# Optimization experiments

Hardware: AMD Instinct MI355X
Metric: run time of the kernel (lower is better)

## Reference

```python
import jax, jax.numpy as jnp
import numpy as np
import math

HEAD_DIM = 128
THETA = 10000.0
MASK_VAL = -10000.0


def _rope(x, cos, sin):
    # x: (B, S, D); cos/sin: (S, D//2). Pairs (even, odd) rotated as complex.
    xr = x.reshape(*x.shape[:-1], -1, 2)
    xe, xo = xr[..., 0], xr[..., 1]
    oe = xe * cos - xo * sin
    oo = xe * sin + xo * cos
    return jnp.stack([oe, oo], axis=-1).reshape(x.shape)


def setup_inputs() -> dict:
    key = jax.random.key(0)
    B, S, D = 8, 4096, HEAD_DIM
    qkv = jax.random.normal(key, (B, S, 3 * D), dtype=jnp.float32)
    return {"qkv": qkv}


def reference(qkv):
    B, S, threeD = qkv.shape
    D = threeD // 3
    qkv = qkv.reshape(B, S, 3, D)
    q, k, v = qkv[:, :, 0], qkv[:, :, 1], qkv[:, :, 2]

    # precompute_freqs_cis: outer(t, 1/theta^(2i/d)) -> cos/sin (S, D//2)
    inv_freq = 1.0 / (THETA ** (jnp.arange(0, D, 2, dtype=jnp.float32) / D))
    freqs = jnp.arange(S, dtype=jnp.float32)[:, None] * inv_freq[None, :]
    cos, sin = jnp.cos(freqs), jnp.sin(freqs)
    q = _rope(q, cos, sin)
    k = _rope(k, cos, sin)

    scale = 1.0 / math.sqrt(D)
    scores = jnp.einsum('btd,bsd->bts', q, k) * scale  # (B, S, S)
    causal_mask = jnp.triu(jnp.full((S, S), MASK_VAL, dtype=scores.dtype), 1)
    attn = jax.nn.softmax(scores + causal_mask, axis=-1)
    out = jnp.einsum('bts,bsd->btd', attn, v)  # (B, S, D)
    return out
```

## Files before the change

kernel.cpp:

```cpp
#include <hip/hip_runtime.h>
#include <math.h>

typedef _Float16 half8 __attribute__((ext_vector_type(8)));
typedef float floatx4 __attribute__((ext_vector_type(4)));
typedef float floatx2 __attribute__((ext_vector_type(2)));

#define B_ 8
#define S_ 4096
#define SCALE_L2E 0.12751743008389106f
#define MASK_L2E  -14426.950408889634f
#define L2_10K_OVER_128 0.10381025296522975f

#define PLD 72
#define KW  136
#define VW  24
#define OSTLD 136
#define SLOTS_PER_B 576
#define NW 8
#define KVTILE 8192

__device__ __forceinline__ int chunk_prefix(int qt32) {
    int g = qt32 >> 4;
    return qt32 + 8 * g * (g - 1) + (qt32 - (g << 4)) * g;
}

__device__ __forceinline__ void glds16(const _Float16* src, _Float16* dst) {
    __builtin_amdgcn_global_load_lds((const __attribute__((address_space(1))) void*)src,
                                     (__attribute__((address_space(3))) void*)dst, 16, 0, 0);
}

__global__ __launch_bounds__(256) void prep_kernel(const float* __restrict__ qkv,
                                                   _Float16* __restrict__ Qh,
                                                   _Float16* __restrict__ Kp,
                                                   _Float16* __restrict__ Vp) {
    __shared__ __align__(16) _Float16 Kl[16][KW];
    __shared__ __align__(16) _Float16 Vt[128][VW];
    const int tid = threadIdx.x;
    const int b   = blockIdx.y;
    const int s0  = blockIdx.x * 16;

#pragma unroll
    for (int it = 0; it < 4; ++it) {
        int idx = tid + it * 256;
        int i = idx & 63, sr = idx >> 6, s = s0 + sr;
        const float* base = qkv + ((size_t)(b * S_ + s)) * 384 + 2 * i;
        floatx2 q2 = *(const floatx2*)base;
        floatx2 k2 = *(const floatx2*)(base + 128);
        float inv = exp2f(-(float)(2 * i) * L2_10K_OVER_128);
        float ang = (float)s * inv;
        float sn, cs;
        __sincosf(ang, &sn, &cs);
        size_t oq = ((size_t)(b * S_ + s)) * 128 + 2 * i;
        Qh[oq]     = (_Float16)((q2[0] * cs - q2[1] * sn) * SCALE_L2E);
        Qh[oq + 1] = (_Float16)((q2[0] * sn + q2[1] * cs) * SCALE_L2E);
        Kl[sr][2 * i]     = (_Float16)(k2[0] * cs - k2[1] * sn);
        Kl[sr][2 * i + 1] = (_Float16)(k2[0] * sn + k2[1] * cs);
    }
#pragma unroll
    for (int it = 0; it < 2; ++it) {
        int idx = tid + it * 256;
        int c = idx & 31, sr = idx >> 5;
        floatx4 v = *(const floatx4*)(qkv + ((size_t)(b * S_ + s0 + sr)) * 384 + 256 + c * 4);
#pragma unroll
        for (int j = 0; j < 4; ++j) Vt[c * 4 + j][sr] = (_Float16)v[j];
    }
    __syncthreads();

    {
        int c = tid >> 6, lane = tid & 63;
        int quad = lane >> 4, n = lane & 15;
        half8 val = *(const half8*)&Kl[n][c * 32 + quad * 8];
        int s16 = s0 >> 4;
        *(half8*)(Kp + (((size_t)(b * 256 + s16) * 4 + c) * 64 + lane) * 8) = val;
    }
    {
        int kt = s0 >> 6, c2 = (s0 >> 5) & 1, qp = (s0 >> 4) & 1;
        int nt = tid >> 5, lq = (tid >> 4) & 1, n = tid & 15;
        int quad = qp * 2 + lq;
        int lane = quad * 16 + n;
        half8 val = *(const half8*)&Vt[nt * 16 + n][lq * 8];
        *(half8*)(Vp + ((((size_t)(b * 64 + kt) * 2 + c2) * 8 + nt) * 64 + lane) * 8) = val;
    }
}

__global__ __launch_bounds__(512) void attn_part_kernel(const _Float16* __restrict__ Qh,
                                                        const _Float16* __restrict__ Kp,
                                                        const _Float16* __restrict__ Vp,
                                                        _Float16* __restrict__ Ppart,
                                                        float* __restrict__ Lpart) {
    __shared__ __align__(16) _Float16 KVs[2][2][KVTILE];
    __shared__ __align__(16) _Float16 Psh[NW][4 * 16 * PLD];

    const int tid  = threadIdx.x;
    const int w    = tid >> 6;
    const int lane = tid & 63;
    const int quad = lane >> 4;
    const int l16  = lane & 15;
    const int b     = blockIdx.x & 7;
    const int chunk = blockIdx.x >> 3;
    const int c0    = chunk * 8;

    const int qt32_top  = 127 - blockIdx.y * 8;
    const int ktmax_blk = (qt32_top * 32 + 31) >> 6;
    if (c0 > ktmax_blk) return;
    const int kend_blk  = min(ktmax_blk, c0 + 7);

    const int qt32   = qt32_top - w;
    const int qr0    = qt32 * 32;
    const int kt_max = (qr0 + 31) >> 6;
    const bool has_work = (c0 <= kt_max);
    const int kend   = min(kt_max, c0 + 7);
    const int slot   = b * SLOTS_PER_B + chunk_prefix(qt32) + chunk;
    _Float16* SHw = &Psh[w][0];

    half8 aq[2][4];
#pragma unroll
    for (int tile = 0; tile < 2; ++tile) {
        const _Float16* Qb = Qh + ((size_t)(b * S_) + qr0 + tile * 16 + l16) * 128;
#pragma unroll
        for (int c = 0; c < 4; ++c) aq[tile][c] = *(const half8*)(Qb + c * 32 + quad * 8);
    }

    floatx4 o[2][8];
#pragma unroll
    for (int tile = 0; tile < 2; ++tile)
#pragma unroll
        for (int i = 0; i < 8; ++i) o[tile][i] = (floatx4){0.f, 0.f, 0.f, 0.f};
    float rsum[2][4] = {{0.f, 0.f, 0.f, 0.f}, {0.f, 0.f, 0.f, 0.f}};

    const _Float16* Kb = Kp + (size_t)b * 524288;
    const _Float16* Vb = Vp + (size_t)b * 524288;

    {
        const _Float16* ks = Kb + (size_t)c0 * KVTILE + (w * 2) * 512 + lane * 8;
        const _Float16* vs = Vb + (size_t)c0 * KVTILE + (w * 2) * 512 + lane * 8;
        _Float16* kd = &KVs[c0 & 1][0][(w * 2) * 512];
        _Float16* vd = &KVs[c0 & 1][1][(w * 2) * 512];
        glds16(ks, kd);       glds16(vs, vd);
        glds16(ks + 512, kd + 512); glds16(vs + 512, vd + 512);
    }

    for (int kt = c0; kt <= kend_blk; ++kt) {
        const int buf = kt & 1;
        if (kt < kend_blk) {
            const _Float16* ks = Kb + (size_t)(kt + 1) * KVTILE + (w * 2) * 512 + lane * 8;
            const _Float16* vs = Vb + (size_t)(kt + 1) * KVTILE + (w * 2) * 512 + lane * 8;
            _Float16* kd = &KVs[buf ^ 1][0][(w * 2) * 512];
            _Float16* vd = &KVs[buf ^ 1][1][(w * 2) * 512];
            glds16(ks, kd);       glds16(vs, vd);
            glds16(ks + 512, kd + 512); glds16(vs + 512, vd + 512);
            asm volatile("s_waitcnt vmcnt(4)" ::: "memory");
        } else {
            asm volatile("s_waitcnt vmcnt(0)" ::: "memory");
        }
        __builtin_amdgcn_s_barrier();

        if (has_work && kt <= kend) {
            const _Float16* Klds = &KVs[buf][0][0];
            const _Float16* Vlds = &KVs[buf][1][0];

            floatx4 s4[2][4];
#pragma unroll
            for (int t = 0; t < 4; ++t) {
                half8 bk[4];
#pragma unroll
                for (int c = 0; c < 4; ++c)
                    bk[c] = *(const half8*)&Klds[((t * 4 + c) * 64 + lane) * 8];
                floatx4 a0 = (floatx4){0.f, 0.f, 0.f, 0.f};
                floatx4 a1 = (floatx4){0.f, 0.f, 0.f, 0.f};
                __builtin_amdgcn_s_setprio(1);
#pragma unroll
                for (int c = 0; c < 4; ++c) {
                    a0 = __builtin_amdgcn_mfma_f32_16x16x32_f16(aq[0][c], bk[c], a0, 0, 0, 0);
                    a1 = __builtin_amdgcn_mfma_f32_16x16x32_f16(aq[1][c], bk[c], a1, 0, 0, 0);
                }
                __builtin_amdgcn_s_setprio(0);
                s4[0][t] = a0; s4[1][t] = a1;
            }

            if (kt == kt_max) {
#pragma unroll
                for (int tile = 0; tile < 2; ++tile)
#pragma unroll
                    for (int t = 0; t < 4; ++t)
#pragma unroll
                        for (int r = 0; r < 4; ++r) {
                            int kcol = kt * 64 + t * 16 + l16;
                            int qr   = qr0 + tile * 16 + quad * 4 + r;
                            if (kcol > qr) s4[tile][t][r] += MASK_L2E;
                        }
            }

#pragma unroll
            for (int tile = 0; tile < 2; ++tile)
#pragma unroll
                for (int t = 0; t < 4; ++t)
#pragma unroll
                    for (int r = 0; r < 4; ++r) {
                        float p = __builtin_amdgcn_exp2f(s4[tile][t][r]);
                        rsum[tile][r] += p;
                        SHw[(tile * 2 + buf) * (16 * PLD) + (quad * 4 + r) * PLD + t * 16 + l16] = (_Float16)p;
                    }

#pragma unroll
            for (int c2 = 0; c2 < 2; ++c2) {
                half8 vf[8];
#pragma unroll
                for (int nt = 0; nt < 8; ++nt)
                    vf[nt] = *(const half8*)&Vlds[((c2 * 8 + nt) * 64 + lane) * 8];
#pragma unroll
                for (int tile = 0; tile < 2; ++tile) {
                    half8 ap = *(const half8*)&SHw[(tile * 2 + buf) * (16 * PLD) + l16 * PLD + c2 * 32 + quad * 8];
                    __builtin_amdgcn_s_setprio(1);
#pragma unroll
                    for (int nt = 0; nt < 8; ++nt)
                        o[tile][nt] = __builtin_amdgcn_mfma_f32_16x16x32_f16(ap, vf[nt], o[tile][nt], 0, 0, 0);
                    __builtin_amdgcn_s_setprio(0);
                }
            }
        }
        asm volatile("" ::: "memory");
        __builtin_amdgcn_s_barrier();
    }

    if (!has_work) return;

#pragma unroll
    for (int off = 1; off <= 8; off <<= 1)
#pragma unroll
        for (int tile = 0; tile < 2; ++tile)
#pragma unroll
            for (int r = 0; r < 4; ++r)
                rsum[tile][r] += __shfl_xor(rsum[tile][r], off, 64);
    if (l16 == 0) {
#pragma unroll
        for (int tile = 0; tile < 2; ++tile)
#pragma unroll
            for (int r = 0; r < 4; ++r)
                Lpart[(size_t)slot * 32 + tile * 16 + quad * 4 + r] = rsum[tile][r];
    }

    _Float16* Ost = SHw;
#pragma unroll
    for (int tile = 0; tile < 2; ++tile)
#pragma unroll
        for (int nt = 0; nt < 8; ++nt)
#pragma unroll
            for (int r = 0; r < 4; ++r)
                Ost[(tile * 16 + quad * 4 + r) * OSTLD + nt * 16 + l16] = (_Float16)o[tile][nt][r];
    _Float16* pp = Ppart + (size_t)slot * 4096;
#pragma unroll
    for (int i = 0; i < 8; ++i) {
        int idx = lane + i * 64;
        half8 v = *(const half8*)&Ost[(idx >> 4) * OSTLD + (idx & 15) * 8];
        *(half8*)(pp + (size_t)idx * 8) = v;
    }
}

__global__ __launch_bounds__(256) void reduce_kernel(const _Float16* __restrict__ Ppart,
                                                     const float* __restrict__ Lpart,
                                                     float* __restrict__ out) {
    const int bid  = blockIdx.x;
    const int b    = bid >> 7;
    const int qt32 = bid & 127;
    const int qr0  = qt32 * 32;
    const int nch  = (((qr0 + 31) >> 6) >> 3) + 1;
    const int slot0 = b * SLOTS_PER_B + chunk_prefix(qt32);
    const _Float16* pp = Ppart + (size_t)slot0 * 4096;
    const float* lp = Lpart + (size_t)slot0 * 32;
    const int tid = threadIdx.x;

#pragma unroll
    for (int j = 0; j < 2; ++j) {
        int idx = tid + j * 256;
        int row = idx >> 4;
        float acc[8] = {0.f, 0.f, 0.f, 0.f, 0.f, 0.f, 0.f, 0.f};
        float l = 0.f;
        for (int c = 0; c < nch; ++c) {
            half8 v = *(const half8*)(pp + (size_t)c * 4096 + (size_t)idx * 8);
#pragma unroll
            for (int k = 0; k < 8; ++k) acc[k] += (float)v[k];
            l += lp[c * 32 + row];
        }
        float inv = 1.0f / l;
        float* ob = out + ((size_t)(b * S_) + qr0) * 128 + (size_t)idx * 8;
        floatx4 o0 = (floatx4){acc[0] * inv, acc[1] * inv, acc[2] * inv, acc[3] * inv};
        floatx4 o1 = (floatx4){acc[4] * inv, acc[5] * inv, acc[6] * inv, acc[7] * inv};
        *(floatx4*)ob = o0;
        *(floatx4*)(ob + 4) = o1;
    }
}

__global__ __launch_bounds__(64) void attn_atomic_kernel(const _Float16* __restrict__ Qh,
                                                         const _Float16* __restrict__ Kp,
                                                         const _Float16* __restrict__ Vp,
                                                         float* __restrict__ out,
                                                         float* __restrict__ Lg) {
    __shared__ __align__(16) _Float16 Pl[2][16 * PLD];
    const int lane = threadIdx.x, quad = lane >> 4, l16 = lane & 15;
    const int b = blockIdx.x & 7, chunk = blockIdx.x >> 3;
    const int qt = 255 - blockIdx.y, qr0 = qt * 16;
    const int kt_max = qt >> 2, c0 = chunk * 8;
    if (c0 > kt_max) return;
    const int kend = min(kt_max, c0 + 7);
    const _Float16* Qb = Qh + ((size_t)(b * S_) + qr0 + l16) * 128;
    half8 aq[4];
#pragma unroll
    for (int c = 0; c < 4; ++c) aq[c] = *(const half8*)(Qb + c * 32 + quad * 8);
    floatx4 o[8];
#pragma unroll
    for (int i = 0; i < 8; ++i) o[i] = (floatx4){0.f, 0.f, 0.f, 0.f};
    float rsum[4] = {0.f, 0.f, 0.f, 0.f};
    const _Float16* Kb = Kp + (size_t)b * 524288;
    const _Float16* Vb = Vp + (size_t)b * 524288;
    for (int kt = c0; kt <= kend; ++kt) {
        half8 vf[2][8];
#pragma unroll
        for (int c2 = 0; c2 < 2; ++c2)
#pragma unroll
            for (int nt = 0; nt < 8; ++nt)
                vf[c2][nt] = *(const half8*)(Vb + (((size_t)(kt * 2 + c2) * 8 + nt) * 64 + lane) * 8);
        floatx4 s4[4];
#pragma unroll
        for (int t = 0; t < 4; ++t) {
            const _Float16* kp = Kb + ((size_t)((kt * 4 + t) * 4) * 64 + lane) * 8;
            floatx4 acc = (floatx4){0.f, 0.f, 0.f, 0.f};
#pragma unroll
            for (int c = 0; c < 4; ++c) {
                half8 bk = *(const half8*)(kp + c * 512);
                acc = __builtin_amdgcn_mfma_f32_16x16x32_f16(aq[c], bk, acc, 0, 0, 0);
            }
            s4[t] = acc;
        }
        if (kt == kt_max) {
#pragma unroll
            for (int t = 0; t < 4; ++t)
#pragma unroll
                for (int r = 0; r < 4; ++r) {
                    int kcol = kt * 64 + t * 16 + l16;
                    int qr = qr0 + quad * 4 + r;
                    if (kcol > qr) s4[t][r] += MASK_L2E;
                }
        }
        const int buf = kt & 1;
#pragma unroll
        for (int t = 0; t < 4; ++t)
#pragma unroll
            for (int r = 0; r < 4; ++r) {
                float p = __builtin_amdgcn_exp2f(s4[t][r]);
                rsum[r] += p;
                Pl[buf][(quad * 4 + r) * PLD + t * 16 + l16] = (_Float16)p;
            }
#pragma unroll
        for (int c2 = 0; c2 < 2; ++c2) {
            half8 ap = *(const half8*)&Pl[buf][l16 * PLD + c2 * 32 + quad * 8];
#pragma unroll
            for (int nt = 0; nt < 8; ++nt)
                o[nt] = __builtin_amdgcn_mfma_f32_16x16x32_f16(ap, vf[c2][nt], o[nt], 0, 0, 0);
        }
    }
#pragma unroll
    for (int off = 1; off <= 8; off <<= 1)
#pragma unroll
        for (int r = 0; r < 4; ++r)
            rsum[r] += __shfl_xor(rsum[r], off, 64);
    if (l16 == 0) {
#pragma unroll
        for (int r = 0; r < 4; ++r)
            atomicAdd(&Lg[(size_t)(b * S_) + qr0 + quad * 4 + r], rsum[r]);
    }
    float* ob = out + ((size_t)(b * S_) + qr0) * 128;
#pragma unroll
    for (int nt = 0; nt < 8; ++nt)
#pragma unroll
        for (int r = 0; r < 4; ++r)
            atomicAdd(&ob[(quad * 4 + r) * 128 + nt * 16 + l16], o[nt][r]);
}

__global__ __launch_bounds__(256) void norm_kernel(float* __restrict__ out,
                                                   const float* __restrict__ Lg) {
    int i = blockIdx.x * 256 + threadIdx.x;
    int row = i >> 5;
    floatx4 v = *(floatx4*)(out + (size_t)i * 4);
    float inv = 1.0f / Lg[row];
    v[0] *= inv; v[1] *= inv; v[2] *= inv; v[3] *= inv;
    *(floatx4*)(out + (size_t)i * 4) = v;
}

extern "C" void kernel_launch(void* const* d_in, const int* in_sizes, int n_in,
                              void* d_out, int out_size, void* d_ws, size_t ws_size,
                              hipStream_t stream) {
    const float* qkv = (const float*)d_in[0];
    float* out = (float*)d_out;
    const size_t MB = 1024 * 1024;
    _Float16* Qh = (_Float16*)d_ws;
    _Float16* Kp = (_Float16*)((char*)d_ws + 8 * MB);
    _Float16* Vp = (_Float16*)((char*)d_ws + 16 * MB);

    const size_t lpart_bytes = (size_t)B_ * SLOTS_PER_B * 32 * sizeof(float);
    const size_t ppart_bytes = (size_t)B_ * SLOTS_PER_B * 4096 * sizeof(_Float16);
    const size_t need = 25 * MB + ppart_bytes;

    prep_kernel<<<dim3(256, B_), dim3(256), 0, stream>>>(qkv, Qh, Kp, Vp);

    if (ws_size >= need) {
        float*    Lpart = (float*)((char*)d_ws + 24 * MB);
        _Float16* Ppart = (_Float16*)((char*)d_ws + 25 * MB);
        (void)lpart_bytes;
        attn_part_kernel<<<dim3(64, 16), dim3(512), 0, stream>>>(Qh, Kp, Vp, Ppart, Lpart);
        reduce_kernel<<<dim3(1024), dim3(256), 0, stream>>>(Ppart, Lpart, out);
    } else {
        float* Lg = (float*)((char*)d_ws + 24 * MB);
        hipMemsetAsync(out, 0, (size_t)B_ * S_ * 128 * sizeof(float), stream);
        hipMemsetAsync(Lg, 0, (size_t)B_ * S_ * sizeof(float), stream);
        attn_atomic_kernel<<<dim3(64, 256), dim3(64), 0, stream>>>(Qh, Kp, Vp, out, Lg);
        norm_kernel<<<dim3(4096), dim3(256), 0, stream>>>(out, Lg);
    }
}
```

Measured before the change: 165.0 us.

## Halve KV tile to 32 keys and pool LDS to raise attention occupancy

Result: no change. 164.7 us (-0.1%).

```diff
diff --git a/kernel.cpp b/kernel.cpp
--- a/kernel.cpp
+++ b/kernel.cpp
@@ -11,13 +11,13 @@
 #define MASK_L2E  -14426.950408889634f
 #define L2_10K_OVER_128 0.10381025296522975f
 
-#define PLD 72
+#define PLD2 40
 #define KW  136
 #define VW  24
 #define OSTLD 136
 #define SLOTS_PER_B 576
 #define NW 8
-#define KVTILE 8192
+#define POOL_HALFS (16384 + NW * 2 * 16 * PLD2)
 
 __device__ __forceinline__ int chunk_prefix(int qt32) {
     int g = qt32 >> 4;
@@ -88,8 +88,7 @@
                                                         const _Float16* __restrict__ Vp,
                                                         _Float16* __restrict__ Ppart,
                                                         float* __restrict__ Lpart) {
-    __shared__ __align__(16) _Float16 KVs[2][2][KVTILE];
-    __shared__ __align__(16) _Float16 Psh[NW][4 * 16 * PLD];
+    __shared__ __align__(16) _Float16 POOL[POOL_HALFS];
 
     const int tid  = threadIdx.x;
     const int w    = tid >> 6;
@@ -111,7 +110,7 @@
     const bool has_work = (c0 <= kt_max);
     const int kend   = min(kt_max, c0 + 7);
     const int slot   = b * SLOTS_PER_B + chunk_prefix(qt32) + chunk;
-    _Float16* SHw = &Psh[w][0];
+    _Float16* Pw = POOL + 16384 + w * (2 * 16 * PLD2);
 
     half8 aq[2][4];
 #pragma unroll
@@ -131,41 +130,42 @@
     const _Float16* Kb = Kp + (size_t)b * 524288;
     const _Float16* Vb = Vp + (size_t)b * 524288;
 
+    const int ht0    = 2 * c0;
+    const int ht_end = 2 * kend_blk + 1;
+
     {
-        const _Float16* ks = Kb + (size_t)c0 * KVTILE + (w * 2) * 512 + lane * 8;
-        const _Float16* vs = Vb + (size_t)c0 * KVTILE + (w * 2) * 512 + lane * 8;
-        _Float16* kd = &KVs[c0 & 1][0][(w * 2) * 512];
-        _Float16* vd = &KVs[c0 & 1][1][(w * 2) * 512];
-        glds16(ks, kd);       glds16(vs, vd);
-        glds16(ks + 512, kd + 512); glds16(vs + 512, vd + 512);
-    }
-
-    for (int kt = c0; kt <= kend_blk; ++kt) {
-        const int buf = kt & 1;
-        if (kt < kend_blk) {
-            const _Float16* ks = Kb + (size_t)(kt + 1) * KVTILE + (w * 2) * 512 + lane * 8;
-            const _Float16* vs = Vb + (size_t)(kt + 1) * KVTILE + (w * 2) * 512 + lane * 8;
-            _Float16* kd = &KVs[buf ^ 1][0][(w * 2) * 512];
-            _Float16* vd = &KVs[buf ^ 1][1][(w * 2) * 512];
-            glds16(ks, kd);       glds16(vs, vd);
-            glds16(ks + 512, kd + 512); glds16(vs + 512, vd + 512);
-            asm volatile("s_waitcnt vmcnt(4)" ::: "memory");
+        const _Float16* ks = Kb + (size_t)ht0 * 4096 + w * 512 + lane * 8;
+        const _Float16* vs = Vb + (size_t)ht0 * 4096 + w * 512 + lane * 8;
+        glds16(ks, POOL + w * 512);
+        glds16(vs, POOL + 4096 + w * 512);
+    }
+
+    for (int ht = ht0; ht <= ht_end; ++ht) {
+        const int buf = ht & 1;
+        if (ht < ht_end) {
+            const _Float16* ks = Kb + (size_t)(ht + 1) * 4096 + w * 512 + lane * 8;
+            const _Float16* vs = Vb + (size_t)(ht + 1) * 4096 + w * 512 + lane * 8;
+            _Float16* kd = POOL + (buf ^ 1) * 8192 + w * 512;
+            glds16(ks, kd);
+            glds16(vs, kd + 4096);
+            asm volatile("s_waitcnt vmcnt(2)" ::: "memory");
         } else {
             asm volatile("s_waitcnt vmcnt(0)" ::: "memory");
         }
         __builtin_amdgcn_s_barrier();
 
+        const int kt = ht >> 1, h = ht & 1;
         if (has_work && kt <= kend) {
-            const _Float16* Klds = &KVs[buf][0][0];
-            const _Float16* Vlds = &KVs[buf][1][0];
-
-            floatx4 s4[2][4];
-#pragma unroll
-            for (int t = 0; t < 4; ++t) {
+            const _Float16* Klds = POOL + buf * 8192;
+            const _Float16* Vlds = Klds + 4096;
+
+            floatx4 s4[2][2];
+#pragma unroll
+            for (int tl = 0; tl < 2; ++tl) {
                 half8 bk[4];
 #pragma unroll
                 for (int c = 0; c < 4; ++c)
-                    bk[c] = *(const half8*)&Klds[((t * 4 + c) * 64 + lane) * 8];
+                    bk[c] = *(const half8*)&Klds[((tl * 4 + c) * 64 + lane) * 8];
                 floatx4 a0 = (floatx4){0.f, 0.f, 0.f, 0.f};
                 floatx4 a1 = (floatx4){0.f, 0.f, 0.f, 0.f};
                 __builtin_amdgcn_s_setprio(1);
@@ -175,42 +175,41 @@
                     a1 = __builtin_amdgcn_mfma_f32_16x16x32_f16(aq[1][c], bk[c], a1, 0, 0, 0);
                 }
                 __builtin_amdgcn_s_setprio(0);
-                s4[0][t] = a0; s4[1][t] = a1;
+                s4[0][tl] = a0; s4[1][tl] = a1;
             }
 
             if (kt == kt_max) {
 #pragma unroll
                 for (int tile = 0; tile < 2; ++tile)
 #pragma unroll
-                    for (int t = 0; t < 4; ++t)
+                    for (int tl = 0; tl < 2; ++tl)
 #pragma unroll
                         for (int r = 0; r < 4; ++r) {
-                            int kcol = kt * 64 + t * 16 + l16;
+                            int kcol = kt * 64 + h * 32 + tl * 16 + l16;
                             int qr   = qr0 + tile * 16 + quad * 4 + r;
-                            if (kcol > qr) s4[tile][t][r] += MASK_L2E;
+                            if (kcol > qr) s4[tile][tl][r] += MASK_L2E;
                         }
             }
 
 #pragma unroll
             for (int tile = 0; tile < 2; ++tile)
 #pragma unroll
-                for (int t = 0; t < 4; ++t)
+                for (int tl = 0; tl < 2; ++tl)
 #pragma unroll
                     for (int r = 0; r < 4; ++r) {
-                        float p = __builtin_amdgcn_exp2f(s4[tile][t][r]);
+                        float p = __builtin_amdgcn_exp2f(s4[tile][tl][r]);
                         rsum[tile][r] += p;
-                        SHw[(tile * 2 + buf) * (16 * PLD) + (quad * 4 + r) * PLD + t * 16 + l16] = (_Float16)p;
+                        Pw[tile * (16 * PLD2) + (quad * 4 + r) * PLD2 + tl * 16 + l16] = (_Float16)p;
                     }
 
-#pragma unroll
-            for (int c2 = 0; c2 < 2; ++c2) {
+            {
                 half8 vf[8];
 #pragma unroll
                 for (int nt = 0; nt < 8; ++nt)
-                    vf[nt] = *(const half8*)&Vlds[((c2 * 8 + nt) * 64 + lane) * 8];
+                    vf[nt] = *(const half8*)&Vlds[(nt * 64 + lane) * 8];
 #pragma unroll
                 for (int tile = 0; tile < 2; ++tile) {
-                    half8 ap = *(const half8*)&SHw[(tile * 2 + buf) * (16 * PLD) + l16 * PLD + c2 * 32 + quad * 8];
+                    half8 ap = *(const half8*)&Pw[tile * (16 * PLD2) + l16 * PLD2 + quad * 8];
                     __builtin_amdgcn_s_setprio(1);
 #pragma unroll
                     for (int nt = 0; nt < 8; ++nt)
@@ -240,20 +239,22 @@
                 Lpart[(size_t)slot * 32 + tile * 16 + quad * 4 + r] = rsum[tile][r];
     }
 
-    _Float16* Ost = SHw;
-#pragma unroll
-    for (int tile = 0; tile < 2; ++tile)
+    asm volatile("" ::: "memory");
+    _Float16* Ost = POOL + w * (POOL_HALFS / NW);
+    _Float16* pp = Ppart + (size_t)slot * 4096;
+#pragma unroll
+    for (int tile = 0; tile < 2; ++tile) {
 #pragma unroll
         for (int nt = 0; nt < 8; ++nt)
 #pragma unroll
             for (int r = 0; r < 4; ++r)
-                Ost[(tile * 16 + quad * 4 + r) * OSTLD + nt * 16 + l16] = (_Float16)o[tile][nt][r];
-    _Float16* pp = Ppart + (size_t)slot * 4096;
-#pragma unroll
-    for (int i = 0; i < 8; ++i) {
-        int idx = lane + i * 64;
-        half8 v = *(const half8*)&Ost[(idx >> 4) * OSTLD + (idx & 15) * 8];
-        *(half8*)(pp + (size_t)idx * 8) = v;
+                Ost[(quad * 4 + r) * OSTLD + nt * 16 + l16] = (_Float16)o[tile][nt][r];
+#pragma unroll
+        for (int i = 0; i < 4; ++i) {
+            int idx = lane + i * 64;
+            half8 v = *(const half8*)&Ost[(idx >> 4) * OSTLD + (idx & 15) * 8];
+            *(half8*)(pp + ((size_t)tile * 256 + idx) * 8) = v;
+        }
     }
 }
 
@@ -291,6 +292,7 @@
     }
 }
 
+#define PLD 72
 __global__ __launch_bounds__(64) void attn_atomic_kernel(const _Float16* __restrict__ Qh,
                                                          const _Float16* __restrict__ Kp,
                                                          const _Float16* __restrict__ Vp,
```
